# Kernel optimization log

Hardware: AMD Instinct MI355X
Metric: run time of the kernel (lower is better)

The kernel has to match this reference:

```python
import jax, jax.numpy as jnp
import numpy as np
from jax import lax

D = 2048
B = 8
T = 1024

def setup_inputs() -> dict:
    key = jax.random.key(0)
    ks = jax.random.split(key, 6)
    s = 1.0 / np.sqrt(D)
    return {
        "x": jax.random.normal(ks[0], (B, T, D), dtype=jnp.float32),
        "h0": jnp.zeros((B, D), dtype=jnp.float32),
        "W_in": jax.random.normal(ks[1], (D, D), dtype=jnp.float32) * s,
        "W_x": jax.random.normal(ks[2], (D, D), dtype=jnp.float32) * s,
        "W_h": jax.random.normal(ks[3], (D, D), dtype=jnp.float32) * (0.5 * s),
        "b": jnp.zeros((D,), dtype=jnp.float32),
        "log_alpha": jnp.asarray(np.log(0.5), dtype=jnp.float32),
        "W_out": jax.random.normal(ks[4], (D, D), dtype=jnp.float32) * s,
    }


def reference(x, h0, W_in, W_x, W_h, b, log_alpha, W_out):
    # x: [B,T,D] -> in_proj + silu pre-activation
    u = jax.nn.silu(jnp.einsum('btd,ed->bte', x, W_in))  # [B,T,D]
    alpha = jnp.exp(log_alpha)
    # Precompute input contribution for all steps: [T,B,D]
    wx_all = jnp.einsum('btd,ed->tbe', u, W_x) + b

    def step(h_prev, wx_t):
        pre = h_prev @ W_h.T + wx_t                  # [B,D]
        h_new = h_prev + alpha * jnp.tanh(pre)
        out = h_new * jax.nn.silu(h_new)             # self-gating
        return h_new, out

    _, outs = lax.scan(step, h0, wx_all)             # outs: [T,B,D]
    y = jnp.einsum('tbd,ed->bte', outs, W_out)       # out_proj -> [B,T,D]
    return y
```

## Files before the change

### kernel.cpp

```cpp
#include <hip/hip_runtime.h>

#define DEV static __device__ __forceinline__

typedef _Float16 half8  __attribute__((ext_vector_type(8)));
typedef _Float16 half4v __attribute__((ext_vector_type(4)));
typedef float    floatx4 __attribute__((ext_vector_type(4)));
typedef unsigned int u32;
typedef unsigned long long u64;
typedef u32 u32x4 __attribute__((ext_vector_type(4)));

#define SPLIT_S 1024.0f
#define SPLIT_R (1.0f / 1024.0f)

DEV void gl_lds16(const _Float16* g, _Float16* l) {
  __builtin_amdgcn_global_load_lds(
      (const __attribute__((address_space(1))) u32*)g,
      (__attribute__((address_space(3))) u32*)l, 16, 0, 0);
}

DEV u32x4 llc_load16(u64 addr) {
  u32x4 r;
  asm volatile("global_load_dwordx4 %0, %1, off sc0 sc1"
               : "=v"(r) : "v"(addr));
  return r;
}
DEV void llc_store8(u64 addr, u64 v) {
  asm volatile("global_store_dwordx2 %0, %1, off sc0 sc1"
               :: "v"(addr), "v"(v) : "memory");
}
DEV void llc_store4(u64 addr, int v) {
  asm volatile("global_store_dword %0, %1, off sc0 sc1"
               :: "v"(addr), "v"(v) : "memory");
}

DEV float fast_tanh(float x) {
  const float e = __expf(2.0f * fabsf(x));
  return copysignf(1.0f - 2.0f / (1.0f + e), x);
}

__global__ __launch_bounds__(256) void k_convert(
    const float* __restrict__ wout, const float* __restrict__ h0,
    _Float16* __restrict__ WoutF, _Float16* __restrict__ hpub,
    int* __restrict__ flags)
{
  if (blockIdx.x == 0 && threadIdx.x < 128) flags[threadIdx.x] = 0;
  const int NW4 = (2048 * 2048) / 4;
  for (int i = blockIdx.x * 256 + threadIdx.x; i < NW4; i += gridDim.x * 256) {
    const float4 v = ((const float4*)wout)[i];
    half4v o;
    o[0] = (_Float16)v.x; o[1] = (_Float16)v.y;
    o[2] = (_Float16)v.z; o[3] = (_Float16)v.w;
    ((half4v*)WoutF)[i] = o;
  }
  for (int i = blockIdx.x * 256 + threadIdx.x; i < 8 * 2048; i += gridDim.x * 256) {
    const float v = h0[i];
    const _Float16 hi = (_Float16)v;
    hpub[i]          = hi;
    hpub[16384 + i]  = (_Float16)((v - (float)hi) * SPLIT_S);
  }
}

template <int EPI>
__global__ __launch_bounds__(256) void k_gemm_split(
    const float* __restrict__ A, const float* __restrict__ B,
    float* __restrict__ C, const float* __restrict__ bias,
    int M, int N, int K)
{
  __shared__ _Float16 Ah[4096], Al[4096], Bh[4096], Bl[4096];
  const int tid  = threadIdx.x;
  const int lane = tid & 63, wave = tid >> 6;
  const int wm = wave >> 1, wn = wave & 1;
  const int tm = blockIdx.y * 128, tn = blockIdx.x * 128;
  const int lr = lane & 15, lk = lane >> 4;

  floatx4 acch[4][4] = {};
  floatx4 accl[4][4] = {};

  for (int k0 = 0; k0 < K; k0 += 32) {
    float4 av[4], bv[4];
#pragma unroll
    for (int q = 0; q < 4; ++q) {
      const int c = tid + q * 256;
      const int rr = c >> 3, cc = (c & 7) * 4;
      av[q] = *(const float4*)(A + (size_t)(tm + rr) * K + k0 + cc);
      bv[q] = *(const float4*)(B + (size_t)(tn + rr) * K + k0 + cc);
    }
    __syncthreads();
#pragma unroll
    for (int q = 0; q < 4; ++q) {
      const int c = tid + q * 256;
      const int rr = c >> 3, cc = (c & 7) * 4;
      half4v ah, al, bh, bl;
#pragma unroll
      for (int j = 0; j < 4; ++j) {
        const float xa = av[q][j], xb = bv[q][j];
        const _Float16 ha = (_Float16)xa, hb = (_Float16)xb;
        ah[j] = ha; al[j] = (_Float16)((xa - (float)ha) * SPLIT_S);
        bh[j] = hb; bl[j] = (_Float16)((xb - (float)hb) * SPLIT_S);
      }
      *(half4v*)(Ah + rr * 32 + cc) = ah;
      *(half4v*)(Al + rr * 32 + cc) = al;
      *(half4v*)(Bh + rr * 32 + cc) = bh;
      *(half4v*)(Bl + rr * 32 + cc) = bl;
    }
    __syncthreads();

    half8 fah[4], fal[4], fbh[4], fbl[4];
#pragma unroll
    for (int mi = 0; mi < 4; ++mi) {
      const int off = (wm * 64 + mi * 16 + lr) * 32 + lk * 8;
      fah[mi] = *(const half8*)(Ah + off);
      fal[mi] = *(const half8*)(Al + off);
    }
#pragma unroll
    for (int ni = 0; ni < 4; ++ni) {
      const int off = (wn * 64 + ni * 16 + lr) * 32 + lk * 8;
      fbh[ni] = *(const half8*)(Bh + off);
      fbl[ni] = *(const half8*)(Bl + off);
    }
#pragma unroll
    for (int mi = 0; mi < 4; ++mi)
#pragma unroll
      for (int ni = 0; ni < 4; ++ni) {
        acch[mi][ni] = __builtin_amdgcn_mfma_f32_16x16x32_f16(fah[mi], fbh[ni], acch[mi][ni], 0, 0, 0);
        accl[mi][ni] = __builtin_amdgcn_mfma_f32_16x16x32_f16(
            fah[mi], fbl[ni],
            __builtin_amdgcn_mfma_f32_16x16x32_f16(fal[mi], fbh[ni], accl[mi][ni], 0, 0, 0),
            0, 0, 0);
      }
  }

#pragma unroll
  for (int mi = 0; mi < 4; ++mi)
#pragma unroll
    for (int ni = 0; ni < 4; ++ni) {
      const int gcol = tn + wn * 64 + ni * 16 + lr;
#pragma unroll
      for (int r = 0; r < 4; ++r) {
        const int grow = tm + wm * 64 + mi * 16 + lk * 4 + r;
        const float v = acch[mi][ni][r] + accl[mi][ni][r] * SPLIT_R;
        if (EPI == 0) {
          C[(size_t)grow * N + gcol] = v / (1.0f + __expf(-v));
        } else {
          const int tt = grow & 1023, bb = grow >> 10;
          C[(size_t)(tt * 8 + bb) * N + gcol] = v + bias[gcol];
        }
      }
    }
}

__global__ __launch_bounds__(256) void k_gemm_out(
    const _Float16* __restrict__ A, const _Float16* __restrict__ B,
    float* __restrict__ C, int M, int N, int K)
{
  __shared__ _Float16 As[4096];
  __shared__ _Float16 Bs[4096];
  const int tid  = threadIdx.x;
  const int lane = tid & 63, wave = tid >> 6;
  const int wm = wave >> 1, wn = wave & 1;
  const int tm = blockIdx.y * 128, tn = blockIdx.x * 128;
  const int lr = lane & 15, lk = lane >> 4;
  const int r0 = tid >> 2;
  const int c0 = (tid & 3) * 8;

  floatx4 acc[4][4] = {};

  for (int k0 = 0; k0 < K; k0 += 32) {
#pragma unroll
    for (int c = 0; c < 2; ++c) {
      const int row = c * 64 + r0;
      gl_lds16(A + (size_t)(tm + row) * K + k0 + c0, As + c * 2048 + wave * 512);
      gl_lds16(B + (size_t)(tn + row) * K + k0 + c0, Bs + c * 2048 + wave * 512);
    }
    __syncthreads();

    half8 af[4], bf[4];
#pragma unroll
    for (int mi = 0; mi < 4; ++mi)
      af[mi] = *(const half8*)(As + (wm * 64 + mi * 16 + lr) * 32 + lk * 8);
#pragma unroll
    for (int ni = 0; ni < 4; ++ni)
      bf[ni] = *(const half8*)(Bs + (wn * 64 + ni * 16 + lr) * 32 + lk * 8);
#pragma unroll
    for (int mi = 0; mi < 4; ++mi)
#pragma unroll
      for (int ni = 0; ni < 4; ++ni)
        acc[mi][ni] = __builtin_amdgcn_mfma_f32_16x16x32_f16(af[mi], bf[ni], acc[mi][ni], 0, 0, 0);
    __syncthreads();
  }

#pragma unroll
  for (int mi = 0; mi < 4; ++mi)
#pragma unroll
    for (int ni = 0; ni < 4; ++ni) {
      const int gcol = tn + wn * 64 + ni * 16 + lr;
#pragma unroll
      for (int r = 0; r < 4; ++r) {
        const int grow = tm + wm * 64 + mi * 16 + lk * 4 + r;
        C[(size_t)grow * N + gcol] = acc[mi][ni][r] * 8.0f;
      }
    }
}

__global__ __launch_bounds__(256, 1) void k_recur(
    const float* __restrict__ Wh, const float* __restrict__ wxp,
    const float* __restrict__ h0p, const float* __restrict__ lalpha,
    _Float16* __restrict__ outs, _Float16* h_pub, int* flags)
{
  __shared__ u32x4 hs4[4096];
  __shared__ float red[256 * 4];
  char* const hs = (char*)hs4;
  const int tid = threadIdx.x;
  const int lane = tid & 63, wave = tid >> 6;
  const int g = blockIdx.x;
  const int e0 = g * 16;
  const int lr = lane & 15, lk = lane >> 4;
  const int lrc = lr & 7;
  const float alpha = __expf(lalpha[0]);

  half8 afh[16], afl[16];
#pragma unroll
  for (int ks = 0; ks < 16; ++ks) {
    const float* wp = Wh + (size_t)(e0 + lr) * 2048 + wave * 512 + ks * 32 + lk * 8;
    const float4 f0 = *(const float4*)wp;
    const float4 f1 = *(const float4*)(wp + 4);
    half8 h, l;
#pragma unroll
    for (int j = 0; j < 4; ++j) {
      const float a0 = ((const float*)&f0)[j], a1 = ((const float*)&f1)[j];
      const _Float16 h0_ = (_Float16)a0;
      const _Float16 h1_ = (_Float16)a1;
      h[j]     = h0_; l[j]     = (_Float16)((a0 - (float)h0_) * SPLIT_S);
      h[j + 4] = h1_; l[j + 4] = (_Float16)((a1 - (float)h1_) * SPLIT_S);
    }
    afh[ks] = h; afl[ks] = l;
  }

  const bool owner = (tid < 64) && (lr < 8);
  float hr0 = 0.f, hr1 = 0.f, hr2 = 0.f, hr3 = 0.f;
  if (owner) {
    const float4 hv = *(const float4*)(h0p + (size_t)lr * 2048 + e0 + lk * 4);
    hr0 = hv.x; hr1 = hv.y; hr2 = hv.z; hr3 = hv.w;
  }

  const u64 hbase = (u64)h_pub;
  const u64 flag_base = (u64)flags;
  const int fb = (lrc * 4096 + (wave * 512 + lk * 8) * 2) ^ (lrc << 4);

  for (int t = 0; t < 1024; ++t) {
    float4 wv = {0.f, 0.f, 0.f, 0.f};
    if (owner) wv = *(const float4*)(wxp + (size_t)(t * 8 + lr) * 2048 + e0 + lk * 4);

    if (t > 0 && wave == 0) {
      const u64* fp = (const u64*)flags + lane;
      for (;;) {
        const u64 fv = __hip_atomic_load(fp, __ATOMIC_RELAXED, __HIP_MEMORY_SCOPE_AGENT);
        if (__all(((int)fv >= t) && ((int)(fv >> 32) >= t))) break;
        __builtin_amdgcn_s_sleep(1);
      }
    }
    __syncthreads();

    const u64 pbase = hbase + (u64)(t & 1) * 65536;

    u32x4 gb[8];
#pragma unroll
    for (int i = 0; i < 8; ++i)
      gb[i] = llc_load16(pbase + (u64)tid * 16 + (u64)i * 4096);
    asm volatile("s_waitcnt vmcnt(0)" ::: "memory");
    __builtin_amdgcn_sched_barrier(0);
#pragma unroll
    for (int i = 0; i < 8; ++i)
      *(u32x4*)(hs + ((tid * 16 + i * 4096) ^ (i << 4))) = gb[i];
    __syncthreads();

    u32x4 gl[8];
#pragma unroll
    for (int i = 0; i < 8; ++i)
      gl[i] = llc_load16(pbase + 32768 + (u64)tid * 16 + (u64)i * 4096);

    floatx4 ph[4] = {};
    floatx4 pl[4] = {};
#pragma unroll
    for (int ks = 0; ks < 16; ++ks) {
      const half8 bh = *(const half8*)(hs + (fb ^ (ks * 64)));
      ph[ks & 3] = __builtin_amdgcn_mfma_f32_16x16x32_f16(afh[ks], bh, ph[ks & 3], 0, 0, 0);
      pl[ks & 3] = __builtin_amdgcn_mfma_f32_16x16x32_f16(afl[ks], bh, pl[ks & 3], 0, 0, 0);
    }

    asm volatile("s_waitcnt vmcnt(0)" ::: "memory");
    __builtin_amdgcn_sched_barrier(0);
#pragma unroll
    for (int i = 0; i < 8; ++i)
      *(u32x4*)(hs + 32768 + ((tid * 16 + i * 4096) ^ (i << 4))) = gl[i];
    __syncthreads();

#pragma unroll
    for (int ks = 0; ks < 16; ++ks) {
      const half8 bl = *(const half8*)(hs + 32768 + (fb ^ (ks * 64)));
      pl[ks & 3] = __builtin_amdgcn_mfma_f32_16x16x32_f16(afh[ks], bl, pl[ks & 3], 0, 0, 0);
    }
    const floatx4 pt = (ph[0] + ph[1] + ph[2] + ph[3]) +
                       (pl[0] + pl[1] + pl[2] + pl[3]) * SPLIT_R;
    *(floatx4*)&red[(wave * 64 + lane) * 4] = pt;
    __syncthreads();

    if (tid < 64) {
      const floatx4* R = (const floatx4*)red;
      const floatx4 s = R[lane] + R[64 + lane] + R[128 + lane] + R[192 + lane];
      union { _Float16 h[4]; u64 u; } hv, lv, ov;
      if (owner) {
        hr0 += alpha * fast_tanh(s[0] + wv.x);
        hr1 += alpha * fast_tanh(s[1] + wv.y);
        hr2 += alpha * fast_tanh(s[2] + wv.z);
        hr3 += alpha * fast_tanh(s[3] + wv.w);
        hv.h[0] = (_Float16)hr0; hv.h[1] = (_Float16)hr1;
        hv.h[2] = (_Float16)hr2; hv.h[3] = (_Float16)hr3;
        lv.h[0] = (_Float16)((hr0 - (float)hv.h[0]) * SPLIT_S);
        lv.h[1] = (_Float16)((hr1 - (float)hv.h[1]) * SPLIT_S);
        lv.h[2] = (_Float16)((hr2 - (float)hv.h[2]) * SPLIT_S);
        lv.h[3] = (_Float16)((hr3 - (float)hv.h[3]) * SPLIT_S);
        const u64 dst = hbase + (u64)((t + 1) & 1) * 65536 +
                        (u64)lr * 4096 + (u64)(e0 + lk * 4) * 2;
        llc_store8(dst,         hv.u);
        llc_store8(dst + 32768, lv.u);
      }
      asm volatile("s_waitcnt vmcnt(0)" ::: "memory");
      if (lane == 0) llc_store4(flag_base + (u64)g * 4, t + 1);
      if (owner) {
        ov.h[0] = (_Float16)((hr0 * hr0 / (1.f + __expf(-hr0))) * 0.125f);
        ov.h[1] = (_Float16)((hr1 * hr1 / (1.f + __expf(-hr1))) * 0.125f);
        ov.h[2] = (_Float16)((hr2 * hr2 / (1.f + __expf(-hr2))) * 0.125f);
        ov.h[3] = (_Float16)((hr3 * hr3 / (1.f + __expf(-hr3))) * 0.125f);
        *(u64*)(outs + (size_t)(lr * 1024 + t) * 2048 + e0 + lk * 4) = ov.u;
      }
    }
  }
}

extern "C" void kernel_launch(void* const* d_in, const int* in_sizes, int n_in,
                              void* d_out, int out_size, void* d_ws, size_t ws_size,
                              hipStream_t stream)
{
  (void)in_sizes; (void)n_in; (void)out_size; (void)ws_size;
  const float* x    = (const float*)d_in[0];
  const float* h0   = (const float*)d_in[1];
  const float* Win  = (const float*)d_in[2];
  const float* Wx   = (const float*)d_in[3];
  const float* Wh   = (const float*)d_in[4];
  const float* bias = (const float*)d_in[5];
  const float* lal  = (const float*)d_in[6];
  const float* Wout = (const float*)d_in[7];

  char* ws = (char*)d_ws;
  float*    U     = (float*)(ws);
  _Float16* OUTS  = (_Float16*)(ws);
  _Float16* WoutF = (_Float16*)(ws + 67108864);
  _Float16* hpub  = (_Float16*)(ws + 75497472);
  int*      flags = (int*)     (ws + 75628544);
  float*    wxbuf = (float*)d_out;

  const dim3 gg(16, 64);

  k_convert<<<512, 256, 0, stream>>>(Wout, h0, WoutF, hpub, flags);
  k_gemm_split<0><<<gg, 256, 0, stream>>>(x, Win, U, nullptr, 8192, 2048, 2048);
  k_gemm_split<1><<<gg, 256, 0, stream>>>(U, Wx, wxbuf, bias, 8192, 2048, 2048);
  k_recur<<<128, 256, 0, stream>>>(Wh, wxbuf, h0, lal, OUTS, hpub, flags);
  k_gemm_out<<<gg, 256, 0, stream>>>(OUTS, WoutF, (float*)d_out, 8192, 2048, 2048);
}
```

Before: 4.629 ms.

## Load published hidden state directly into MFMA registers, dropping LDS staging

Changes the global layout of the published h buffer to a fragment-major order, 8-column chunks with batches interleaved, so each lane can load its MFMA B-operand fragments straight from the LLC. This removes the LDS staging, the swizzled stores and two block-wide barriers per timestep in the serial recurrence. Each wave now issues 32 loads instead of 16 and all waves read the whole h vector redundantly, trading more global traffic for fewer synchronisation points. The h0 initialisation and the per-step store addresses are updated to match the new layout.

```diff
diff --git a/kernel.cpp b/kernel.cpp
--- a/kernel.cpp
+++ b/kernel.cpp
@@ -40,7 +40,7 @@
 
 __global__ __launch_bounds__(256) void k_convert(
     const float* __restrict__ wout, const float* __restrict__ h0,
-    _Float16* __restrict__ WoutF, _Float16* __restrict__ hpub,
+    _Float16* __restrict__ WoutF, char* __restrict__ hpub,
     int* __restrict__ flags)
 {
   if (blockIdx.x == 0 && threadIdx.x < 128) flags[threadIdx.x] = 0;
@@ -52,11 +52,18 @@
     o[2] = (_Float16)v.z; o[3] = (_Float16)v.w;
     ((half4v*)WoutF)[i] = o;
   }
-  for (int i = blockIdx.x * 256 + threadIdx.x; i < 8 * 2048; i += gridDim.x * 256) {
-    const float v = h0[i];
-    const _Float16 hi = (_Float16)v;
-    hpub[i]          = hi;
-    hpub[16384 + i]  = (_Float16)((v - (float)hi) * SPLIT_S);
+  for (int id = blockIdx.x * 256 + threadIdx.x; id < 2048; id += gridDim.x * 256) {
+    const int c = id >> 3, b = id & 7;
+    union { _Float16 h[8]; u32x4 v; } hi, lo;
+#pragma unroll
+    for (int j = 0; j < 8; ++j) {
+      const float v = h0[b * 2048 + c * 8 + j];
+      const _Float16 h = (_Float16)v;
+      hi.h[j] = h;
+      lo.h[j] = (_Float16)((v - (float)h) * SPLIT_S);
+    }
+    *(u32x4*)(hpub + c * 128 + b * 16)         = hi.v;
+    *(u32x4*)(hpub + 32768 + c * 128 + b * 16) = lo.v;
   }
 }
 
@@ -205,11 +212,9 @@
 __global__ __launch_bounds__(256, 1) void k_recur(
     const float* __restrict__ Wh, const float* __restrict__ wxp,
     const float* __restrict__ h0p, const float* __restrict__ lalpha,
-    _Float16* __restrict__ outs, _Float16* h_pub, int* flags)
-{
-  __shared__ u32x4 hs4[4096];
+    _Float16* __restrict__ outs, char* __restrict__ h_pub, int* flags)
+{
   __shared__ float red[256 * 4];
-  char* const hs = (char*)hs4;
   const int tid = threadIdx.x;
   const int lane = tid & 63, wave = tid >> 6;
   const int g = blockIdx.x;
@@ -245,7 +250,7 @@
 
   const u64 hbase = (u64)h_pub;
   const u64 flag_base = (u64)flags;
-  const int fb = (lrc * 4096 + (wave * 512 + lk * 8) * 2) ^ (lrc << 4);
+  const u64 gb_off = (u64)((wave * 64 + lk) * 128 + lrc * 16);
 
   for (int t = 0; t < 1024; ++t) {
     float4 wv = {0.f, 0.f, 0.f, 0.f};
@@ -261,43 +266,29 @@
     }
     __syncthreads();
 
-    const u64 pbase = hbase + (u64)(t & 1) * 65536;
-
-    u32x4 gb[8];
-#pragma unroll
-    for (int i = 0; i < 8; ++i)
-      gb[i] = llc_load16(pbase + (u64)tid * 16 + (u64)i * 4096);
+    const u64 pb = hbase + (u64)(t & 1) * 65536 + gb_off;
+    u32x4 sh[16], sl[16];
+#pragma unroll
+    for (int ks = 0; ks < 16; ++ks) sh[ks] = llc_load16(pb + (u64)ks * 512);
+#pragma unroll
+    for (int ks = 0; ks < 16; ++ks) sl[ks] = llc_load16(pb + 32768 + (u64)ks * 512);
+    asm volatile("s_waitcnt vmcnt(16)" ::: "memory");
+    __builtin_amdgcn_sched_barrier(0);
+
+    floatx4 ph[4] = {};
+    floatx4 pl[4] = {};
+#pragma unroll
+    for (int ks = 0; ks < 16; ++ks) {
+      const half8 bh = __builtin_bit_cast(half8, sh[ks]);
+      ph[ks & 3] = __builtin_amdgcn_mfma_f32_16x16x32_f16(afh[ks], bh, ph[ks & 3], 0, 0, 0);
+      pl[ks & 3] = __builtin_amdgcn_mfma_f32_16x16x32_f16(afl[ks], bh, pl[ks & 3], 0, 0, 0);
+    }
     asm volatile("s_waitcnt vmcnt(0)" ::: "memory");
     __builtin_amdgcn_sched_barrier(0);
-#pragma unroll
-    for (int i = 0; i < 8; ++i)
-      *(u32x4*)(hs + ((tid * 16 + i * 4096) ^ (i << 4))) = gb[i];
-    __syncthreads();
-
-    u32x4 gl[8];
-#pragma unroll
-    for (int i = 0; i < 8; ++i)
-      gl[i] = llc_load16(pbase + 32768 + (u64)tid * 16 + (u64)i * 4096);
-
-    floatx4 ph[4] = {};
-    floatx4 pl[4] = {};
+
 #pragma unroll
     for (int ks = 0; ks < 16; ++ks) {
-      const half8 bh = *(const half8*)(hs + (fb ^ (ks * 64)));
-      ph[ks & 3] = __builtin_amdgcn_mfma_f32_16x16x32_f16(afh[ks], bh, ph[ks & 3], 0, 0, 0);
-      pl[ks & 3] = __builtin_amdgcn_mfma_f32_16x16x32_f16(afl[ks], bh, pl[ks & 3], 0, 0, 0);
-    }
-
-    asm volatile("s_waitcnt vmcnt(0)" ::: "memory");
-    __builtin_amdgcn_sched_barrier(0);
-#pragma unroll
-    for (int i = 0; i < 8; ++i)
-      *(u32x4*)(hs + 32768 + ((tid * 16 + i * 4096) ^ (i << 4))) = gl[i];
-    __syncthreads();
-
-#pragma unroll
-    for (int ks = 0; ks < 16; ++ks) {
-      const half8 bl = *(const half8*)(hs + 32768 + (fb ^ (ks * 64)));
+      const half8 bl = __builtin_bit_cast(half8, sl[ks]);
       pl[ks & 3] = __builtin_amdgcn_mfma_f32_16x16x32_f16(afh[ks], bl, pl[ks & 3], 0, 0, 0);
     }
     const floatx4 pt = (ph[0] + ph[1] + ph[2] + ph[3]) +
@@ -321,7 +312,7 @@
         lv.h[2] = (_Float16)((hr2 - (float)hv.h[2]) * SPLIT_S);
         lv.h[3] = (_Float16)((hr3 - (float)hv.h[3]) * SPLIT_S);
         const u64 dst = hbase + (u64)((t + 1) & 1) * 65536 +
-                        (u64)lr * 4096 + (u64)(e0 + lk * 4) * 2;
+                        (u64)((2 * g + (lk >> 1)) * 128 + lr * 16 + (lk & 1) * 8);
         llc_store8(dst,         hv.u);
         llc_store8(dst + 32768, lv.u);
       }
@@ -356,8 +347,8 @@
   float*    U     = (float*)(ws);
   _Float16* OUTS  = (_Float16*)(ws);
   _Float16* WoutF = (_Float16*)(ws + 67108864);
-  _Float16* hpub  = (_Float16*)(ws + 75497472);
-  int*      flags = (int*)     (ws + 75628544);
+  char*     hpub  = ws + 75497472;
+  int*      flags = (int*)(ws + 75628544);
   float*    wxbuf = (float*)d_out;
 
   const dim3 gg(16, 64);
```

After: 4.513 ms. 1.03x faster.
